# Kernel optimization log

Measured on AMD Instinct MI355X. Metric: run time of the kernel, lower is better.

## Reference

```python
import jax, jax.numpy as jnp
import numpy as np

B = 4096
DETER = 2048
BLOCKS = 8
HIDDEN = 256
SC, SD = 32, 16
STOCH = SC * SD  # 512
ACT = 17
EMBED = 1024
UNIMIX = 0.01
EPS = 1e-4
DPB = DETER // BLOCKS  # 256


def rmsnorm(x, scale):
    rms = jnp.sqrt(jnp.mean(x * x, axis=-1, keepdims=True) + EPS)
    return x / rms * scale


def dense(x, w, b):
    return x @ w + b


def block_linear(x, kernel, bias):
    # kernel: (out_per_block, in_per_block, blocks)
    bs = x.shape[:-1]
    ipb = x.shape[-1] // BLOCKS
    xg = x.reshape(*bs, BLOCKS, ipb)
    y = jnp.einsum('...gi,oig->...go', xg, kernel)
    return y.reshape(*bs, -1) + bias


def sample(logits):
    # unimix + straight-through argmax
    probs = jax.nn.softmax(logits, axis=-1)
    probs = (1.0 - UNIMIX) * probs + UNIMIX / SD
    logits = jnp.log(probs + 1e-8)
    soft = jax.nn.softmax(logits, axis=-1)
    hard = jax.nn.one_hot(jnp.argmax(logits, axis=-1), SD, dtype=soft.dtype)
    return hard + soft - jax.lax.stop_gradient(soft)


def setup_inputs() -> dict:
    key = jax.random.key(0)
    ks = jax.random.split(key, 16)

    def lecun(k, shape, fan_in):
        return jax.random.normal(k, shape, jnp.float32) / np.sqrt(fan_in)

    return {
        'stoch': jax.random.uniform(ks[0], (B, SC, SD), jnp.float32),
        'deter': jax.random.normal(ks[1], (B, DETER), jnp.float32),
        'action': jax.random.normal(ks[2], (B, ACT), jnp.float32),
        'embed': jax.random.normal(ks[3], (B, EMBED), jnp.float32),
        # Deter net params
        'in0_w': lecun(ks[4], (DETER, HIDDEN), DETER), 'in0_b': jnp.zeros((HIDDEN,)), 'in_norm0_s': jnp.ones((HIDDEN,)),
        'in1_w': lecun(ks[5], (STOCH, HIDDEN), STOCH), 'in1_b': jnp.zeros((HIDDEN,)), 'in_norm1_s': jnp.ones((HIDDEN,)),
        'in2_w': lecun(ks[6], (ACT, HIDDEN), ACT), 'in2_b': jnp.zeros((HIDDEN,)), 'in_norm2_s': jnp.ones((HIDDEN,)),
        'hid0_k': lecun(ks[7], (DPB, DPB + 3 * HIDDEN, BLOCKS), DPB + 3 * HIDDEN),
        'hid0_b': jnp.zeros((DETER,)), 'hid_norm0_s': jnp.ones((DETER,)),
        'gru_k': lecun(ks[8], (3 * DPB, DPB, BLOCKS), DPB), 'gru_b': jnp.zeros((3 * DETER,)),
        # posterior head
        'obs_fc0_w': lecun(ks[9], (DETER + EMBED, HIDDEN), DETER + EMBED), 'obs_fc0_b': jnp.zeros((HIDDEN,)),
        'obs_norm0_s': jnp.ones((HIDDEN,)),
        'obs_out_w': lecun(ks[10], (HIDDEN, STOCH), HIDDEN), 'obs_out_b': jnp.zeros((STOCH,)),
    }


def reference(stoch, deter, action, embed,
              in0_w, in0_b, in_norm0_s, in1_w, in1_b, in_norm1_s,
              in2_w, in2_b, in_norm2_s, hid0_k, hid0_b, hid_norm0_s,
              gru_k, gru_b, obs_fc0_w, obs_fc0_b, obs_norm0_s,
              obs_out_w, obs_out_b):
    Bn = stoch.shape[0]
    stoch_flat = stoch.reshape(Bn, -1)  # (B, 512)
    act = action / jnp.maximum(jnp.abs(action), 1.0)
    x0 = jax.nn.silu(rmsnorm(dense(deter, in0_w, in0_b), in_norm0_s))
    x1 = jax.nn.silu(rmsnorm(dense(stoch_flat, in1_w, in1_b), in_norm1_s))
    x2 = jax.nn.silu(rmsnorm(dense(act, in2_w, in2_b), in_norm2_s))
    x = jnp.concatenate([x0, x1, x2], axis=-1)  # (B, 768)
    x = jnp.broadcast_to(x[:, None, :], (Bn, BLOCKS, x.shape[-1]))
    deter_blocked = deter.reshape(Bn, BLOCKS, DPB)
    x = jnp.concatenate([deter_blocked, x], axis=-1).reshape(Bn, -1)  # (B, 8192)
    x = jax.nn.silu(rmsnorm(block_linear(x, hid0_k, hid0_b), hid_norm0_s))  # (B, 2048)
    gates = block_linear(x, gru_k, gru_b)  # (B, 6144)
    gates = gates.reshape(Bn, BLOCKS, 3 * DPB)
    g0, g1, g2 = jnp.split(gates, 3, axis=-1)
    reset = jax.nn.sigmoid(g0.reshape(Bn, -1))
    cand = g1.reshape(Bn, -1)
    update = jax.nn.sigmoid(g2.reshape(Bn, -1) - 1.0)
    new_deter = update * jnp.tanh(reset * cand) + (1.0 - update) * deter
    # posterior head
    h = jnp.concatenate([new_deter, embed], axis=-1)
    h = jax.nn.silu(rmsnorm(dense(h, obs_fc0_w, obs_fc0_b), obs_norm0_s))
    logit = dense(h, obs_out_w, obs_out_b).reshape(Bn, SC, SD)
    new_stoch = sample(logit)
    return (new_stoch, new_deter, logit)
```

## Files before the change

### kernel.cpp

```cpp
#include <hip/hip_runtime.h>
#include <cmath>

constexpr int BATCH = 4096;
constexpr float EPSN = 1e-4f;

constexpr int OFF_STOCH = 0;
constexpr int OFF_DETER = BATCH * 512;
constexpr int OFF_LOGIT = OFF_DETER + BATCH * 2048;

typedef unsigned short ushort;
typedef __attribute__((ext_vector_type(4))) float f32x4;
typedef __attribute__((ext_vector_type(8))) short s16x8;
struct us4 { ushort x, y, z, w; };

constexpr size_t U_WHH = 0;
constexpr size_t U_WHL = U_WHH + 2097152;
constexpr size_t U_WGH = U_WHL + 2097152;
constexpr size_t U_WGL = U_WGH + 1572864;
constexpr size_t U_WFH = U_WGL + 1572864;
constexpr size_t U_WFL = U_WFH + 786432;
constexpr size_t U_WOH = U_WFL + 786432;
constexpr size_t U_WOL = U_WOH + 131072;
constexpr size_t U_PEND = U_WOL + 131072;
constexpr size_t F_XB = U_PEND / 2;
constexpr size_t F_XH = F_XB + 3145728;
constexpr size_t U_X0H = (F_XH + 6291456) * 2;
constexpr size_t U_X0L = U_X0H + 524288;
constexpr size_t U_X1H = U_X0L + 524288;
constexpr size_t U_X1L = U_X1H + 131072;
constexpr size_t F_HB = F_XH + 4194304;

#define DINLINE __device__ __forceinline__

DINLINE float sigm(float x)  { return 1.0f / (1.0f + expf(-x)); }
DINLINE float siluf(float x) { return x / (1.0f + expf(-x)); }

DINLINE float4 ld4(const float* p) { return *reinterpret_cast<const float4*>(p); }
DINLINE void st4(float* p, float4 v) { *reinterpret_cast<float4*>(p) = v; }

DINLINE ushort f2bf(float x) {
  unsigned u = __float_as_uint(x);
  unsigned r = u + 0x7fffu + ((u >> 16) & 1u);
  return (ushort)(r >> 16);
}
DINLINE float bf2f(ushort h) { return __uint_as_float(((unsigned)h) << 16); }

DINLINE void cp16g(void* lds, const void* g) {
  __builtin_amdgcn_global_load_lds(
      (const __attribute__((address_space(1))) unsigned int*)g,
      (__attribute__((address_space(3))) unsigned int*)lds, 16, 0, 0);
}

DINLINE f32x4 mfma16(s16x8 a, s16x8 b, f32x4 c) {
  return __builtin_amdgcn_mfma_f32_16x16x32_bf16(a, b, c, 0, 0, 0);
}

DINLINE int swz_addr(int row, int kb0) {
  return (row * 64 + kb0) ^ ((row & 7) << 4);
}
DINLINE void dec_swz(int D, int& row, int& kb) {
  int r2 = (D >> 8) & 1;
  int r0 = ((D >> 6) & 1) ^ r2;
  row = ((D >> 7) << 1) | r0;
  kb = (D & 48) ^ ((row & 3) << 4);
}

DINLINE void split2(float x, ushort& h, ushort& l) {
  h = f2bf(x);
  l = f2bf(x - bf2f(h));
}

DINLINE float4 rms_silu4(float v0, float v1, float v2, float v3, float4 s4) {
  float ss = v0 * v0 + v1 * v1 + v2 * v2 + v3 * v3;
#pragma unroll
  for (int off = 32; off; off >>= 1) ss += __shfl_xor(ss, off);
  float inv = 1.0f / sqrtf(ss * (1.0f / 256.0f) + EPSN);
  float4 o;
  o.x = siluf(v0 * inv * s4.x); o.y = siluf(v1 * inv * s4.y);
  o.z = siluf(v2 * inv * s4.z); o.w = siluf(v3 * inv * s4.w);
  return o;
}

__global__ __launch_bounds__(256) void k_prep(
    const float* __restrict__ hk, const float* __restrict__ gk,
    const float* __restrict__ w0, const float* __restrict__ w1,
    const float* __restrict__ wf, const float* __restrict__ wo,
    ushort* __restrict__ wsU) {
  __shared__ float L[64 * 65];
  const int bid = blockIdx.x, tid = threadIdx.x;
  if (bid < 1792) {
    int t = bid * 256 + tid;
    const float* src; ushort* dh; ushort* dl; int e, plane;
    if (t < 262144) { e = t; src = hk + (size_t)e * 8; dh = wsU + U_WHH; dl = wsU + U_WHL; plane = 262144; }
    else { e = t - 262144; src = gk + (size_t)e * 8; dh = wsU + U_WGH; dl = wsU + U_WGL; plane = 196608; }
    float4 v0 = ld4(src), v1 = ld4(src + 4);
    float vv[8] = {v0.x, v0.y, v0.z, v0.w, v1.x, v1.y, v1.z, v1.w};
#pragma unroll
    for (int g2 = 0; g2 < 8; ++g2) {
      ushort h, l; split2(vv[g2], h, l);
      dh[(size_t)g2 * plane + e] = h;
      dl[(size_t)g2 * plane + e] = l;
    }
    return;
  }
  int t = bid - 1792;
  const float* src; ushort* dh; ushort* dl; int K, N;
  if (t < 128)      { src = w0; dh = wsU + U_X0H; dl = wsU + U_X0L; K = 2048; N = 256; }
  else if (t < 160) { t -= 128; src = w1; dh = wsU + U_X1H; dl = wsU + U_X1L; K = 512;  N = 256; }
  else if (t < 352) { t -= 160; src = wf; dh = wsU + U_WFH; dl = wsU + U_WFL; K = 3072; N = 256; }
  else              { t -= 352; src = wo; dh = wsU + U_WOH; dl = wsU + U_WOL; K = 256;  N = 512; }
  const int ntiles = N / 64;
  const int k0 = (t / ntiles) * 64, n0 = (t % ntiles) * 64;
#pragma unroll
  for (int q = 0; q < 4; ++q) {
    int row = q * 16 + (tid >> 4), col = (tid & 15) * 4;
    float4 v = ld4(src + (size_t)(k0 + row) * N + n0 + col);
    L[row * 65 + col]     = v.x;
    L[row * 65 + col + 1] = v.y;
    L[row * 65 + col + 2] = v.z;
    L[row * 65 + col + 3] = v.w;
  }
  __syncthreads();
  const int n = tid >> 2, kc = (tid & 3) * 16;
  s16x8 h0, h1, l0v, l1v;
#pragma unroll
  for (int j = 0; j < 16; ++j) {
    ushort h, l; split2(L[(kc + j) * 65 + n], h, l);
    if (j < 8) { h0[j] = (short)h; l0v[j] = (short)l; }
    else       { h1[j - 8] = (short)h; l1v[j - 8] = (short)l; }
  }
  size_t ob = (size_t)(n0 + n) * K + k0 + kc;
  *(s16x8*)(dh + ob)     = h0;
  *(s16x8*)(dh + ob + 8) = h1;
  *(s16x8*)(dl + ob)     = l0v;
  *(s16x8*)(dl + ob + 8) = l1v;
}

__global__ __launch_bounds__(512) void k_gemm256(
    int mode,
    const float* __restrict__ deter, const float* __restrict__ stoch,
    const float* __restrict__ newdet, const float* __restrict__ embed,
    const ushort* __restrict__ wsU, float* __restrict__ part) {
  __shared__ ushort Ah[2][64 * 32], Al[2][64 * 32];
  __shared__ ushort Wh[2][256 * 32], Wl[2][256 * 32];
  const int tid = threadIdx.x, lane = tid & 63, wv = tid >> 6;
  const int wr = wv >> 2, wc = wv & 3;
  const int bid = blockIdx.x;
  constexpr size_t PL0 = (size_t)4096 * 512;

  const float* A0; const float* A1 = nullptr;
  int lda0, lda1 = 0, ksw = 1 << 30;
  const ushort* whp; const ushort* wlp;
  int KwB, kbase, KT, m0, dstride, dcol;
  float* dst;

  if (mode == 0) {
    if (bid < 256) {
      int ks = bid & 3; m0 = (bid >> 2) * 64; kbase = ks * 512; KT = 16;
      A0 = deter; lda0 = 2048;
      whp = wsU + U_X0H; wlp = wsU + U_X0L; KwB = 4096;
      dst = part + (size_t)(ks >> 1) * PL0; dstride = 512; dcol = (ks & 1) * 256;
    } else {
      int b = bid - 256; int ks = b & 1; m0 = (b >> 1) * 64; kbase = ks * 256; KT = 8;
      A0 = stoch; lda0 = 512;
      whp = wsU + U_X1H; wlp = wsU + U_X1L; KwB = 1024;
      dst = part + 2 * PL0; dstride = 512; dcol = ks * 256;
    }
  } else {
    int ks = bid & 3; m0 = (bid >> 2) * 64; kbase = ks * 768; KT = 24;
    A0 = newdet; lda0 = 2048; A1 = embed; lda1 = 1024; ksw = 2048;
    whp = wsU + U_WFH; wlp = wsU + U_WFL; KwB = 6144;
    dst = part + (size_t)ks * 4096 * 256; dstride = 256; dcol = 0;
  }

  int wn0, wkb0, wn1, wkb1;
  dec_swz(tid * 16, wn0, wkb0);
  dec_swz(8192 + tid * 16, wn1, wkb1);
  const char* whB = (const char*)whp;
  const char* wlB = (const char*)wlp;
  const size_t wo0 = (size_t)wn0 * KwB + kbase * 2 + wkb0;
  const size_t wo1 = (size_t)wn1 * KwB + kbase * 2 + wkb1;

  const int arow = tid >> 2, akq = (tid & 3) * 8;
  const int abyte = swz_addr(arow, (tid & 3) * 16);
  float av[8];

  const f32x4 z4 = {0.f, 0.f, 0.f, 0.f};
  f32x4 acc[2][4];
#pragma unroll
  for (int i = 0; i < 2; ++i)
#pragma unroll
    for (int j = 0; j < 4; ++j) acc[i][j] = z4;

#define U_LOADA(kt) \
  if (tid < 256) { \
    int kg = kbase + (kt) * 32 + akq; \
    const float* p = (kg < ksw) ? A0 + (size_t)(m0 + arow) * lda0 + kg \
                                : A1 + (size_t)(m0 + arow) * lda1 + (kg - ksw); \
    float4 u_ = ld4(p), w_ = ld4(p + 4); \
    av[0] = u_.x; av[1] = u_.y; av[2] = u_.z; av[3] = u_.w; \
    av[4] = w_.x; av[5] = w_.y; av[6] = w_.z; av[7] = w_.w; \
  }
#define U_WRITEA(buf) \
  if (tid < 256) { \
    s16x8 h8, l8; \
    _Pragma("unroll") \
    for (int j = 0; j < 8; ++j) { \
      ushort h_, l_; split2(av[j], h_, l_); \
      h8[j] = (short)h_; l8[j] = (short)l_; \
    } \
    *(s16x8*)((char*)Ah[buf] + abyte) = h8; \
    *(s16x8*)((char*)Al[buf] + abyte) = l8; \
  }
#define U_ISSUEW(buf, kt) { \
    cp16g((char*)Wh[buf] + tid * 16, whB + wo0 + (kt) * 64); \
    cp16g((char*)Wh[buf] + 8192 + tid * 16, whB + wo1 + (kt) * 64); \
    cp16g((char*)Wl[buf] + tid * 16, wlB + wo0 + (kt) * 64); \
    cp16g((char*)Wl[buf] + 8192 + tid * 16, wlB + wo1 + (kt) * 64); \
  }

  U_LOADA(0);
  U_ISSUEW(0, 0);
  U_WRITEA(0);
  __syncthreads();
  int cur = 0;
  for (int t = 0; t < KT; ++t) {
    if (t + 1 < KT) { U_ISSUEW(cur ^ 1, t + 1); U_LOADA(t + 1); }
    const int k16 = (lane >> 4) * 16;
    s16x8 afh[2], afl[2];
#pragma unroll
    for (int mf = 0; mf < 2; ++mf) {
      int by = swz_addr(wr * 32 + mf * 16 + (lane & 15), k16);
      afh[mf] = *(const s16x8*)((const char*)Ah[cur] + by);
      afl[mf] = *(const s16x8*)((const char*)Al[cur] + by);
    }
#pragma unroll
    for (int nf = 0; nf < 4; ++nf) {
      int by = swz_addr(wc * 64 + nf * 16 + (lane & 15), k16);
      s16x8 bh = *(const s16x8*)((const char*)Wh[cur] + by);
      s16x8 bl = *(const s16x8*)((const char*)Wl[cur] + by);
#pragma unroll
      for (int mf = 0; mf < 2; ++mf) {
        acc[mf][nf] = mfma16(afh[mf], bh, acc[mf][nf]);
        acc[mf][nf] = mfma16(afh[mf], bl, acc[mf][nf]);
        acc[mf][nf] = mfma16(afl[mf], bh, acc[mf][nf]);
      }
    }
    if (t + 1 < KT) { U_WRITEA(cur ^ 1); }
    __syncthreads();
    cur ^= 1;
  }
#undef U_LOADA
#undef U_WRITEA
#undef U_ISSUEW
#pragma unroll
  for (int mf = 0; mf < 2; ++mf) {
    int rbase = m0 + wr * 32 + mf * 16 + ((lane >> 4) << 2);
#pragma unroll
    for (int nf = 0; nf < 4; ++nf) {
      int col = dcol + wc * 64 + nf * 16 + (lane & 15);
#pragma unroll
      for (int r = 0; r < 4; ++r)
        dst[(size_t)(rbase + r) * dstride + col] = acc[mf][nf][r];
    }
  }
}

__global__ __launch_bounds__(512) void k_x2(
    const float* __restrict__ action, const float* __restrict__ w2,
    const float* __restrict__ b2, const float* __restrict__ s2,
    ushort* __restrict__ xbp) {
  __shared__ float W2s[17 * 256];
  __shared__ float A2s[128 * 20];
  const int tid = threadIdx.x, tx = tid & 63, wv = tid >> 6;
  const int m0 = blockIdx.x * 128;
  for (int e = tid; e < 17 * 256; e += 512) W2s[e] = w2[e];
  for (int e = tid; e < 128 * 17; e += 512) {
    int r = e / 17, c = e % 17;
    float a = action[(size_t)(m0 + r) * 17 + c];
    float m = fabsf(a);
    A2s[r * 20 + c] = a / (m > 1.f ? m : 1.f);
  }
  __syncthreads();
  float4 acc2[16];
#pragma unroll
  for (int r = 0; r < 16; ++r) acc2[r] = make_float4(0.f, 0.f, 0.f, 0.f);
#pragma unroll
  for (int k = 0; k < 17; ++k) {
    float4 w4 = ld4(W2s + k * 256 + tx * 4);
#pragma unroll
    for (int r = 0; r < 16; ++r) {
      float av = A2s[(wv * 16 + r) * 20 + k];
      acc2[r].x = fmaf(av, w4.x, acc2[r].x);
      acc2[r].y = fmaf(av, w4.y, acc2[r].y);
      acc2[r].z = fmaf(av, w4.z, acc2[r].z);
      acc2[r].w = fmaf(av, w4.w, acc2[r].w);
    }
  }
  float4 b4 = ld4(b2 + tx * 4);
  float4 s4 = ld4(s2 + tx * 4);
#pragma unroll
  for (int r = 0; r < 16; ++r) {
    float4 o = rms_silu4(acc2[r].x + b4.x, acc2[r].y + b4.y,
                         acc2[r].z + b4.z, acc2[r].w + b4.w, s4);
    us4 h4, l4;
    split2(o.x, h4.x, l4.x); split2(o.y, h4.y, l4.y);
    split2(o.z, h4.z, l4.z); split2(o.w, h4.w, l4.w);
    size_t rb = (size_t)(m0 + wv * 16 + r) * 1536;
    *(us4*)(xbp + rb + 512 + tx * 4) = h4;
    *(us4*)(xbp + rb + 768 + 512 + tx * 4) = l4;
  }
}

__global__ __launch_bounds__(256) void k_comb_in(
    const float* __restrict__ part,
    const float* __restrict__ b0, const float* __restrict__ s0,
    const float* __restrict__ b1, const float* __restrict__ s1,
    ushort* __restrict__ xbp) {
  const int tid = threadIdx.x, tx = tid & 63, wv = tid >> 6;
  const size_t row = blockIdx.x * 2 + (wv >> 1);
  const int half = wv & 1;
  constexpr size_t PL = (size_t)4096 * 512;
  float4 v = make_float4(0.f, 0.f, 0.f, 0.f);
  if (half == 0) {
#pragma unroll
    for (int p = 0; p < 2; ++p) {
      const float* s = part + p * PL + row * 512 + tx * 4;
      float4 a = ld4(s), b = ld4(s + 256);
      v.x += a.x + b.x; v.y += a.y + b.y; v.z += a.z + b.z; v.w += a.w + b.w;
    }
  } else {
    const float* s = part + 2 * PL + row * 512 + tx * 4;
    float4 a = ld4(s), b = ld4(s + 256);
    v.x = a.x + b.x; v.y = a.y + b.y; v.z = a.z + b.z; v.w = a.w + b.w;
  }
  const float* bp = half ? b1 : b0;
  const float* sp = half ? s1 : s0;
  float4 b4 = ld4(bp + tx * 4);
  float4 s4 = ld4(sp + tx * 4);
  float4 o = rms_silu4(v.x + b4.x, v.y + b4.y, v.z + b4.z, v.w + b4.w, s4);
  us4 h4, l4;
  split2(o.x, h4.x, l4.x); split2(o.y, h4.y, l4.y);
  split2(o.z, h4.z, l4.z); split2(o.w, h4.w, l4.w);
  *(us4*)(xbp + row * 1536 + half * 256 + tx * 4) = h4;
  *(us4*)(xbp + row * 1536 + 768 + half * 256 + tx * 4) = l4;
}

__global__ __launch_bounds__(256) void k_comb4(
    const float* __restrict__ part, const float* __restrict__ bias,
    const float* __restrict__ scale, ushort* __restrict__ hbp) {
  const int tid = threadIdx.x, tx = tid & 63, wv = tid >> 6;
  const size_t row = blockIdx.x * 4 + wv;
  float4 v = make_float4(0.f, 0.f, 0.f, 0.f);
#pragma unroll
  for (int ks = 0; ks < 4; ++ks) {
    float4 t = ld4(part + (size_t)ks * 4096 * 256 + row * 256 + tx * 4);
    v.x += t.x; v.y += t.y; v.z += t.z; v.w += t.w;
  }
  float4 b4 = ld4(bias + tx * 4);
  float4 s4 = ld4(scale + tx * 4);
  float4 o = rms_silu4(v.x + b4.x, v.y + b4.y, v.z + b4.z, v.w + b4.w, s4);
  us4 h4, l4;
  split2(o.x, h4.x, l4.x); split2(o.y, h4.y, l4.y);
  split2(o.z, h4.z, l4.z); split2(o.w, h4.w, l4.w);
  *(us4*)(hbp + row * 512 + tx * 4) = h4;
  *(us4*)(hbp + row * 512 + 256 + tx * 4) = l4;
}

__global__ __launch_bounds__(512) void k_hid0m(
    const float* __restrict__ deter, const ushort* __restrict__ xbp,
    const ushort* __restrict__ wsU,
    const float* __restrict__ hbias, float* __restrict__ yh) {
  __shared__ ushort Ah[2][64 * 32], Al[2][64 * 32];
  __shared__ ushort Wh[2][256 * 32], Wl[2][256 * 32];
  const int tid = threadIdx.x, lane = tid & 63, wv = tid >> 6;
  const int wr = wv >> 2, wc = wv & 3;
  const int g = blockIdx.x & 7;
  const int m0 = (int)(blockIdx.x >> 3) * 64;

  int wn0, wkb0, wn1, wkb1;
  dec_swz(tid * 16, wn0, wkb0);
  dec_swz(8192 + tid * 16, wn1, wkb1);
  const char* whhB = (const char*)(wsU + U_WHH) + (size_t)g * 256 * 2048;
  const char* whlB = (const char*)(wsU + U_WHL) + (size_t)g * 256 * 2048;
  const char* xbB = (const char*)xbp;

  const int arow = tid >> 2, akq = (tid & 3) * 8;
  const int abyte = swz_addr(arow, (tid & 3) * 16);
  int an0, akb;
  dec_swz(tid * 16, an0, akb);
  float av[8];

  const f32x4 z4 = {0.f, 0.f, 0.f, 0.f};
  f32x4 acc[2][4];
#pragma unroll
  for (int i = 0; i < 2; ++i)
#pragma unroll
    for (int j = 0; j < 4; ++j) acc[i][j] = z4;

#define H_LOADA_DET(kt) \
  if (tid < 256) { \
    const float* p = deter + (size_t)(m0 + arow) * 2048 + g * 256 + (kt) * 32 + akq; \
    float4 u_ = ld4(p), w_ = ld4(p + 4); \
    av[0] = u_.x; av[1] = u_.y; av[2] = u_.z; av[3] = u_.w; \
    av[4] = w_.x; av[5] = w_.y; av[6] = w_.z; av[7] = w_.w; \
  }
#define H_WRITEA(buf) \
  if (tid < 256) { \
    s16x8 h8, l8; \
    _Pragma("unroll") \
    for (int j = 0; j < 8; ++j) { \
      ushort h_, l_; split2(av[j], h_, l_); \
      h8[j] = (short)h_; l8[j] = (short)l_; \
    } \
    *(s16x8*)((char*)Ah[buf] + abyte) = h8; \
    *(s16x8*)((char*)Al[buf] + abyte) = l8; \
  }
#define H_ISSUEA(buf, kt) \
  if (tid < 256) { \
    size_t rb = (size_t)(m0 + an0) * 3072; \
    int co = ((kt) * 32 - 256) * 2 + akb; \
    cp16g((char*)Ah[buf] + tid * 16, xbB + rb + co); \
    cp16g((char*)Al[buf] + tid * 16, xbB + rb + 1536 + co); \
  }
#define H_ISSUEW(buf, kt) { \
    size_t o0_ = (size_t)wn0 * 2048 + (kt) * 64 + wkb0; \
    size_t o1_ = (size_t)wn1 * 2048 + (kt) * 64 + wkb1; \
    cp16g((char*)Wh[buf] + tid * 16, whhB + o0_); \
    cp16g((char*)Wh[buf] + 8192 + tid * 16, whhB + o1_); \
    cp16g((char*)Wl[buf] + tid * 16, whlB + o0_); \
    cp16g((char*)Wl[buf] + 8192 + tid * 16, whlB + o1_); \
  }

  H_LOADA_DET(0);
  H_ISSUEW(0, 0);
  H_WRITEA(0);
  __syncthreads();
  int cur = 0;
  for (int t = 0; t < 32; ++t) {
    const bool pf = (t + 1 < 32);
    const bool det = (t + 1 < 8);
    if (pf) {
      H_ISSUEW(cur ^ 1, t + 1);
      if (det) { H_LOADA_DET(t + 1); }
      else     { H_ISSUEA(cur ^ 1, t + 1); }
    }
    const int k16 = (lane >> 4) * 16;
    s16x8 afh[2], afl[2];
#pragma unroll
    for (int mf = 0; mf < 2; ++mf) {
      int by = swz_addr(wr * 32 + mf * 16 + (lane & 15), k16);
      afh[mf] = *(const s16x8*)((const char*)Ah[cur] + by);
      afl[mf] = *(const s16x8*)((const char*)Al[cur] + by);
    }
#pragma unroll
    for (int nf = 0; nf < 4; ++nf) {
      int by = swz_addr(wc * 64 + nf * 16 + (lane & 15), k16);
      s16x8 bh = *(const s16x8*)((const char*)Wh[cur] + by);
      s16x8 bl = *(const s16x8*)((const char*)Wl[cur] + by);
#pragma unroll
      for (int mf = 0; mf < 2; ++mf) {
        acc[mf][nf] = mfma16(afh[mf], bh, acc[mf][nf]);
        acc[mf][nf] = mfma16(afh[mf], bl, acc[mf][nf]);
        acc[mf][nf] = mfma16(afl[mf], bh, acc[mf][nf]);
      }
    }
    if (pf && det) { H_WRITEA(cur ^ 1); }
    __syncthreads();
    cur ^= 1;
  }
#undef H_LOADA_DET
#undef H_WRITEA
#undef H_ISSUEA
#undef H_ISSUEW
#pragma unroll
  for (int mf = 0; mf < 2; ++mf) {
    int rbase = m0 + wr * 32 + mf * 16 + ((lane >> 4) << 2);
#pragma unroll
    for (int nf = 0; nf < 4; ++nf) {
      int col = wc * 64 + nf * 16 + (lane & 15);
      float b = hbias[g * 256 + col];
#pragma unroll
      for (int r = 0; r < 4; ++r)
        yh[(size_t)(rbase + r) * 2048 + g * 256 + col] = acc[mf][nf][r] + b;
    }
  }
}

__global__ __launch_bounds__(256) void k_rmsnorm2048(
    float* __restrict__ xh, const float* __restrict__ scale) {
  const int b = blockIdx.x, tid = threadIdx.x;
  float* row = xh + (size_t)b * 2048;
  float4 v0 = ld4(row + tid * 8);
  float4 v1 = ld4(row + tid * 8 + 4);
  float ss = v0.x * v0.x + v0.y * v0.y + v0.z * v0.z + v0.w * v0.w +
             v1.x * v1.x + v1.y * v1.y + v1.z * v1.z + v1.w * v1.w;
#pragma unroll
  for (int off = 32; off; off >>= 1) ss += __shfl_xor(ss, off);
  __shared__ float wsum[4];
  if ((tid & 63) == 0) wsum[tid >> 6] = ss;
  __syncthreads();
  float tot = wsum[0] + wsum[1] + wsum[2] + wsum[3];
  float inv = 1.0f / sqrtf(tot * (1.0f / 2048.0f) + EPSN);
  float4 sc0 = ld4(scale + tid * 8);
  float4 sc1 = ld4(scale + tid * 8 + 4);
  float o[8];
  o[0] = siluf(v0.x * inv * sc0.x); o[1] = siluf(v0.y * inv * sc0.y);
  o[2] = siluf(v0.z * inv * sc0.z); o[3] = siluf(v0.w * inv * sc0.w);
  o[4] = siluf(v1.x * inv * sc1.x); o[5] = siluf(v1.y * inv * sc1.y);
  o[6] = siluf(v1.z * inv * sc1.z); o[7] = siluf(v1.w * inv * sc1.w);
  s16x8 h8, l8;
#pragma unroll
  for (int j = 0; j < 8; ++j) {
    ushort h, l; split2(o[j], h, l);
    h8[j] = (short)h; l8[j] = (short)l;
  }
  ushort* rp = (ushort*)row;
  *(s16x8*)(rp + tid * 8) = h8;
  *(s16x8*)(rp + 2048 + tid * 8) = l8;
}

__global__ __launch_bounds__(512) void k_grum(
    const ushort* __restrict__ xhp, const ushort* __restrict__ wsU,
    const float* __restrict__ gb, const float* __restrict__ deter,
    float* __restrict__ newdet) {
  __shared__ ushort Ah[2][128 * 32], Al[2][128 * 32];
  __shared__ ushort Wh[2][192 * 32], Wl[2][192 * 32];
  const int tid = threadIdx.x, lane = tid & 63, wv = tid >> 6;
  const int wr = wv >> 2, wc = wv & 3;
  const int g = blockIdx.x & 7;
  const int nc = (int)(blockIdx.x >> 3) & 3;
  const int m0 = (int)(blockIdx.x >> 5) * 128;

  int wn0, wkb0, wn1, wkb1;
  dec_swz(tid * 16, wn0, wkb0);
  dec_swz(8192 + tid * 16, wn1, wkb1);
  const char* wghB = (const char*)(wsU + U_WGH);
  const char* wglB = (const char*)(wsU + U_WGL);
  const size_t wo0 = (size_t)(g * 768 + ((wn0 >> 6) << 8) + nc * 64 + (wn0 & 63)) * 512 + wkb0;
  const size_t wo1 = (size_t)(g * 768 + ((wn1 >> 6) << 8) + nc * 64 + (wn1 & 63)) * 512 + wkb1;

  const char* xhB = (const char*)xhp;
  int an0, akb;
  dec_swz(tid * 16, an0, akb);

  const f32x4 z4 = {0.f, 0.f, 0.f, 0.f};
  f32x4 acc[4][3];
#pragma unroll
  for (int i = 0; i < 4; ++i)
#pragma unroll
    for (int j = 0; j < 3; ++j) acc[i][j] = z4;

#define G_ISSUEA(buf, kt) { \
    size_t rb = (size_t)(m0 + an0) * 8192; \
    int co = (g * 256 + (kt) * 32) * 2 + akb; \
    cp16g((char*)Ah[buf] + tid * 16, xhB + rb + co); \
    cp16g((char*)Al[buf] + tid * 16, xhB + rb + 4096 + co); \
  }
#define G_ISSUEW(buf, kt) { \
    cp16g((char*)Wh[buf] + tid * 16, wghB + wo0 + (kt) * 64); \
    cp16g((char*)Wl[buf] + tid * 16, wglB + wo0 + (kt) * 64); \
    if (tid < 256) { \
      cp16g((char*)Wh[buf] + 8192 + tid * 16, wghB + wo1 + (kt) * 64); \
      cp16g((char*)Wl[buf] + 8192 + tid * 16, wglB + wo1 + (kt) * 64); \
    } }

  G_ISSUEW(0, 0);
  G_ISSUEA(0, 0);
  __syncthreads();
  int cur = 0;
  for (int t = 0; t < 8; ++t) {
    if (t + 1 < 8) { G_ISSUEW(cur ^ 1, t + 1); G_ISSUEA(cur ^ 1, t + 1); }
    const int k16 = (lane >> 4) * 16;
    s16x8 afh[4], afl[4];
#pragma unroll
    for (int mf = 0; mf < 4; ++mf) {
      int by = swz_addr(wr * 64 + mf * 16 + (lane & 15), k16);
      afh[mf] = *(const s16x8*)((const char*)Ah[cur] + by);
      afl[mf] = *(const s16x8*)((const char*)Al[cur] + by);
    }
#pragma unroll
    for (int gt = 0; gt < 3; ++gt) {
      int by = swz_addr(gt * 64 + wc * 16 + (lane & 15), k16);
      s16x8 bh = *(const s16x8*)((const char*)Wh[cur] + by);
      s16x8 bl = *(const s16x8*)((const char*)Wl[cur] + by);
#pragma unroll
      for (int mf = 0; mf < 4; ++mf) {
        acc[mf][gt] = mfma16(afh[mf], bh, acc[mf][gt]);
        acc[mf][gt] = mfma16(afh[mf], bl, acc[mf][gt]);
        acc[mf][gt] = mfma16(afl[mf], bh, acc[mf][gt]);
      }
    }
    __syncthreads();
    cur ^= 1;
  }
#undef G_ISSUEA
#undef G_ISSUEW
  const int col = nc * 64 + wc * 16 + (lane & 15);
  const float br = gb[g * 768 + col];
  const float bc = gb[g * 768 + 256 + col];
  const float bu = gb[g * 768 + 512 + col];
#pragma unroll
  for (int mf = 0; mf < 4; ++mf) {
    int rbase = m0 + wr * 64 + mf * 16 + ((lane >> 4) << 2);
#pragma unroll
    for (int r = 0; r < 4; ++r) {
      int row = rbase + r;
      float rr = sigm(acc[mf][0][r] + br);
      float cc = acc[mf][1][r] + bc;
      float uu = sigm(acc[mf][2][r] + bu - 1.0f);
      float d = deter[(size_t)row * 2048 + g * 256 + col];
      newdet[(size_t)row * 2048 + g * 256 + col] =
          uu * tanhf(rr * cc) + (1.0f - uu) * d;
    }
  }
}

__global__ __launch_bounds__(512) void k_obsoutm(
    const ushort* __restrict__ hbp, const ushort* __restrict__ wsU,
    const float* __restrict__ ob, float* __restrict__ logit) {
  __shared__ ushort Ah[2][64 * 32], Al[2][64 * 32];
  __shared__ ushort Wh[2][256 * 32], Wl[2][256 * 32];
  const int tid = threadIdx.x, lane = tid & 63, wv = tid >> 6;
  const int wr = wv >> 2, wc = wv & 3;
  const int half = blockIdx.x & 1;
  const int m0 = (int)(blockIdx.x >> 1) * 64;

  int wn0, wkb0, wn1, wkb1;
  dec_swz(tid * 16, wn0, wkb0);
  dec_swz(8192 + tid * 16, wn1, wkb1);
  const char* whB = (const char*)(wsU + U_WOH) + (size_t)half * 256 * 512;
  const char* wlB = (const char*)(wsU + U_WOL) + (size_t)half * 256 * 512;
  const size_t wo0 = (size_t)wn0 * 512 + wkb0;
  const size_t wo1 = (size_t)wn1 * 512 + wkb1;

  const char* hbB = (const char*)hbp;
  int an0, akb;
  dec_swz(tid * 16, an0, akb);

  const f32x4 z4 = {0.f, 0.f, 0.f, 0.f};
  f32x4 acc[2][4];
#pragma unroll
  for (int i = 0; i < 2; ++i)
#pragma unroll
    for (int j = 0; j < 4; ++j) acc[i][j] = z4;

#define O_ISSUEA(buf, kt) \
  if (tid < 256) { \
    size_t rb = (size_t)(m0 + an0) * 1024; \
    int co = (kt) * 64 + akb; \
    cp16g((char*)Ah[buf] + tid * 16, hbB + rb + co); \
    cp16g((char*)Al[buf] + tid * 16, hbB + rb + 512 + co); \
  }
#define O_ISSUEW(buf, kt) { \
    cp16g((char*)Wh[buf] + tid * 16, whB + wo0 + (kt) * 64); \
    cp16g((char*)Wh[buf] + 8192 + tid * 16, whB + wo1 + (kt) * 64); \
    cp16g((char*)Wl[buf] + tid * 16, wlB + wo0 + (kt) * 64); \
    cp16g((char*)Wl[buf] + 8192 + tid * 16, wlB + wo1 + (kt) * 64); \
  }

  O_ISSUEW(0, 0);
  O_ISSUEA(0, 0);
  __syncthreads();
  int cur = 0;
  for (int t = 0; t < 8; ++t) {
    if (t + 1 < 8) { O_ISSUEW(cur ^ 1, t + 1); O_ISSUEA(cur ^ 1, t + 1); }
    const int k16 = (lane >> 4) * 16;
    s16x8 afh[2], afl[2];
#pragma unroll
    for (int mf = 0; mf < 2; ++mf) {
      int by = swz_addr(wr * 32 + mf * 16 + (lane & 15), k16);
      afh[mf] = *(const s16x8*)((const char*)Ah[cur] + by);
      afl[mf] = *(const s16x8*)((const char*)Al[cur] + by);
    }
#pragma unroll
    for (int nf = 0; nf < 4; ++nf) {
      int by = swz_addr(wc * 64 + nf * 16 + (lane & 15), k16);
      s16x8 bh = *(const s16x8*)((const char*)Wh[cur] + by);
      s16x8 bl = *(const s16x8*)((const char*)Wl[cur] + by);
#pragma unroll
      for (int mf = 0; mf < 2; ++mf) {
        acc[mf][nf] = mfma16(afh[mf], bh, acc[mf][nf]);
        acc[mf][nf] = mfma16(afh[mf], bl, acc[mf][nf]);
        acc[mf][nf] = mfma16(afl[mf], bh, acc[mf][nf]);
      }
    }
    __syncthreads();
    cur ^= 1;
  }
#undef O_ISSUEA
#undef O_ISSUEW
#pragma unroll
  for (int mf = 0; mf < 2; ++mf) {
    int rbase = m0 + wr * 32 + mf * 16 + ((lane >> 4) << 2);
#pragma unroll
    for (int nf = 0; nf < 4; ++nf) {
      int col = half * 256 + wc * 64 + nf * 16 + (lane & 15);
      float b = ob[col];
#pragma unroll
      for (int r = 0; r < 4; ++r)
        logit[(size_t)(rbase + r) * 512 + col] = acc[mf][nf][r] + b;
    }
  }
}

__global__ __launch_bounds__(256) void k_argmax(
    const float* __restrict__ logit, float* __restrict__ stoch_out) {
  const size_t row = blockIdx.x * 4 + (threadIdx.x >> 6);
  const int lane = threadIdx.x & 63;
  const float* lp = logit + row * 512 + lane * 8;
  float4 a = ld4(lp), b = ld4(lp + 4);
  float v[8] = {a.x, a.y, a.z, a.w, b.x, b.y, b.z, b.w};
  float bv = v[0]; int bi = 0;
#pragma unroll
  for (int j = 1; j < 8; ++j)
    if (v[j] > bv) { bv = v[j]; bi = j; }
  bi += lane * 8;
  float pv = __shfl_xor(bv, 1);
  int   pi = __shfl_xor(bi, 1);
  if (pv > bv || (pv == bv && pi < bi)) { bv = pv; bi = pi; }
  float4 o0, o1;
  int base = lane * 8;
  o0.x = (bi == base + 0) ? 1.f : 0.f;
  o0.y = (bi == base + 1) ? 1.f : 0.f;
  o0.z = (bi == base + 2) ? 1.f : 0.f;
  o0.w = (bi == base + 3) ? 1.f : 0.f;
  o1.x = (bi == base + 4) ? 1.f : 0.f;
  o1.y = (bi == base + 5) ? 1.f : 0.f;
  o1.z = (bi == base + 6) ? 1.f : 0.f;
  o1.w = (bi == base + 7) ? 1.f : 0.f;
  st4(stoch_out + row * 512 + base, o0);
  st4(stoch_out + row * 512 + base + 4, o1);
}

extern "C" void kernel_launch(void* const* d_in, const int* in_sizes, int n_in,
                              void* d_out, int out_size, void* d_ws, size_t ws_size,
                              hipStream_t stream) {
  (void)in_sizes; (void)n_in; (void)out_size; (void)ws_size;
  const float* stoch      = (const float*)d_in[0];
  const float* deter      = (const float*)d_in[1];
  const float* action     = (const float*)d_in[2];
  const float* embed      = (const float*)d_in[3];
  const float* in0_w      = (const float*)d_in[4];
  const float* in0_b      = (const float*)d_in[5];
  const float* n0_s       = (const float*)d_in[6];
  const float* in1_w      = (const float*)d_in[7];
  const float* in1_b      = (const float*)d_in[8];
  const float* n1_s       = (const float*)d_in[9];
  const float* in2_w      = (const float*)d_in[10];
  const float* in2_b      = (const float*)d_in[11];
  const float* n2_s       = (const float*)d_in[12];
  const float* hid0_k     = (const float*)d_in[13];
  const float* hid0_b     = (const float*)d_in[14];
  const float* hidn_s     = (const float*)d_in[15];
  const float* gru_k      = (const float*)d_in[16];
  const float* gru_b      = (const float*)d_in[17];
  const float* obs_fc0_w  = (const float*)d_in[18];
  const float* obs_fc0_b  = (const float*)d_in[19];
  const float* obs_n_s    = (const float*)d_in[20];
  const float* obs_out_w  = (const float*)d_in[21];
  const float* obs_out_b  = (const float*)d_in[22];

  float*  out = (float*)d_out;
  float*  ws  = (float*)d_ws;
  ushort* wsU = (ushort*)d_ws;
  ushort* xbp = (ushort*)(ws + F_XB);
  float*  xh  = ws + F_XH;
  ushort* xhp = (ushort*)(ws + F_XH);
  ushort* hbp = (ushort*)(ws + F_HB);
  float*  part = xh;

  hipLaunchKernelGGL(k_prep, dim3(2176), dim3(256), 0, stream,
                     hid0_k, gru_k, in0_w, in1_w, obs_fc0_w, obs_out_w, wsU);
  hipLaunchKernelGGL(k_x2, dim3(32), dim3(512), 0, stream,
                     action, in2_w, in2_b, n2_s, xbp);
  hipLaunchKernelGGL(k_gemm256, dim3(384), dim3(512), 0, stream,
                     0, deter, stoch, out + OFF_DETER, embed, wsU, part);
  hipLaunchKernelGGL(k_comb_in, dim3(2048), dim3(256), 0, stream,
                     part, in0_b, n0_s, in1_b, n1_s, xbp);
  hipLaunchKernelGGL(k_hid0m, dim3(512), dim3(512), 0, stream,
                     deter, xbp, wsU, hid0_b, xh);
  hipLaunchKernelGGL(k_rmsnorm2048, dim3(4096), dim3(256), 0, stream, xh, hidn_s);
  hipLaunchKernelGGL(k_grum, dim3(1024), dim3(512), 0, stream,
                     xhp, wsU, gru_b, deter, out + OFF_DETER);
  hipLaunchKernelGGL(k_gemm256, dim3(256), dim3(512), 0, stream,
                     1, deter, stoch, out + OFF_DETER, embed, wsU, part);
  hipLaunchKernelGGL(k_comb4, dim3(1024), dim3(256), 0, stream,
                     part, obs_fc0_b, obs_n_s, hbp);
  hipLaunchKernelGGL(k_obsoutm, dim3(128), dim3(512), 0, stream,
                     hbp, wsU, obs_out_b, out + OFF_LOGIT);
  hipLaunchKernelGGL(k_argmax, dim3(1024), dim3(256), 0, stream,
                     out + OFF_LOGIT, out + OFF_STOCH);
}
```

Before: 241.2 us.

## Pre-swizzle weights into MFMA fragment order and load B directly from global

The prep kernel now writes all bf16 hi/lo weight planes in an MFMA-fragment-major layout, so each lane's 16-byte B fragment sits contiguously in global memory. The GEMM kernels drop the shared-memory weight staging buffers and async copies and load B fragments straight into registers each k-step. This removes LDS traffic and shrinks shared memory use, which may raise occupancy. In exchange, weight loads are no longer double-buffered ahead of use, so global/L2 latency may show up inside the MFMA loop.

Measured after the change: 258.1 us. 7.0% more time.

```diff
diff --git a/kernel.cpp b/kernel.cpp
--- a/kernel.cpp
+++ b/kernel.cpp
@@ -70,6 +70,10 @@
   l = f2bf(x - bf2f(h));
 }
 
+DINLINE size_t frag_idx(int n, int k, int NK) {
+  return ((size_t)((n >> 4) * NK + (k >> 5)) * 64 + ((k >> 3) & 3) * 16 + (n & 15)) * 8 + (k & 7);
+}
+
 DINLINE float4 rms_silu4(float v0, float v1, float v2, float v3, float4 s4) {
   float ss = v0 * v0 + v1 * v1 + v2 * v2 + v3 * v3;
 #pragma unroll
@@ -90,16 +94,33 @@
   const int bid = blockIdx.x, tid = threadIdx.x;
   if (bid < 1792) {
     int t = bid * 256 + tid;
-    const float* src; ushort* dh; ushort* dl; int e, plane;
-    if (t < 262144) { e = t; src = hk + (size_t)e * 8; dh = wsU + U_WHH; dl = wsU + U_WHL; plane = 262144; }
-    else { e = t - 262144; src = gk + (size_t)e * 8; dh = wsU + U_WGH; dl = wsU + U_WGL; plane = 196608; }
-    float4 v0 = ld4(src), v1 = ld4(src + 4);
-    float vv[8] = {v0.x, v0.y, v0.z, v0.w, v1.x, v1.y, v1.z, v1.w};
-#pragma unroll
-    for (int g2 = 0; g2 < 8; ++g2) {
-      ushort h, l; split2(vv[g2], h, l);
-      dh[(size_t)g2 * plane + e] = h;
-      dl[(size_t)g2 * plane + e] = l;
+    if (t < 262144) {
+      int o = t >> 10, i = t & 1023;
+      const float* src = hk + (size_t)t * 8;
+      float4 v0 = ld4(src), v1 = ld4(src + 4);
+      float vv[8] = {v0.x, v0.y, v0.z, v0.w, v1.x, v1.y, v1.z, v1.w};
+      size_t fi = frag_idx(o, i, 32);
+#pragma unroll
+      for (int g2 = 0; g2 < 8; ++g2) {
+        ushort h, l; split2(vv[g2], h, l);
+        wsU[U_WHH + (size_t)g2 * 262144 + fi] = h;
+        wsU[U_WHL + (size_t)g2 * 262144 + fi] = l;
+      }
+    } else {
+      int e = t - 262144;
+      int o = e >> 8, i = e & 255;
+      const float* src = gk + (size_t)e * 8;
+      float4 v0 = ld4(src), v1 = ld4(src + 4);
+      float vv[8] = {v0.x, v0.y, v0.z, v0.w, v1.x, v1.y, v1.z, v1.w};
+      int gate = o >> 8, nc = (o >> 6) & 3, srow = gate * 64 + (o & 63);
+      size_t fi = frag_idx(srow, i, 8);
+#pragma unroll
+      for (int g2 = 0; g2 < 8; ++g2) {
+        ushort h, l; split2(vv[g2], h, l);
+        size_t pb = (size_t)(g2 * 4 + nc) * 49152;
+        wsU[U_WGH + pb + fi] = h;
+        wsU[U_WGL + pb + fi] = l;
+      }
     }
     return;
   }
@@ -109,6 +130,7 @@
   else if (t < 160) { t -= 128; src = w1; dh = wsU + U_X1H; dl = wsU + U_X1L; K = 512;  N = 256; }
   else if (t < 352) { t -= 160; src = wf; dh = wsU + U_WFH; dl = wsU + U_WFL; K = 3072; N = 256; }
   else              { t -= 352; src = wo; dh = wsU + U_WOH; dl = wsU + U_WOL; K = 256;  N = 512; }
+  const int NK = K / 32;
   const int ntiles = N / 64;
   const int k0 = (t / ntiles) * 64, n0 = (t % ntiles) * 64;
 #pragma unroll
@@ -121,19 +143,21 @@
     L[row * 65 + col + 3] = v.w;
   }
   __syncthreads();
-  const int n = tid >> 2, kc = (tid & 3) * 16;
+  const int nl = tid >> 2, kc = (tid & 3) * 16;
+  const int ng = n0 + nl;
   s16x8 h0, h1, l0v, l1v;
 #pragma unroll
   for (int j = 0; j < 16; ++j) {
-    ushort h, l; split2(L[(kc + j) * 65 + n], h, l);
+    ushort h, l; split2(L[(kc + j) * 65 + nl], h, l);
     if (j < 8) { h0[j] = (short)h; l0v[j] = (short)l; }
     else       { h1[j - 8] = (short)h; l1v[j - 8] = (short)l; }
   }
-  size_t ob = (size_t)(n0 + n) * K + k0 + kc;
-  *(s16x8*)(dh + ob)     = h0;
-  *(s16x8*)(dh + ob + 8) = h1;
-  *(s16x8*)(dl + ob)     = l0v;
-  *(s16x8*)(dl + ob + 8) = l1v;
+  size_t fa = frag_idx(ng, k0 + kc, NK);
+  size_t fb = frag_idx(ng, k0 + kc + 8, NK);
+  *(s16x8*)(dh + fa) = h0;
+  *(s16x8*)(dh + fb) = h1;
+  *(s16x8*)(dl + fa) = l0v;
+  *(s16x8*)(dl + fb) = l1v;
 }
 
 __global__ __launch_bounds__(512) void k_gemm256(
@@ -142,7 +166,6 @@
     const float* __restrict__ newdet, const float* __restrict__ embed,
     const ushort* __restrict__ wsU, float* __restrict__ part) {
   __shared__ ushort Ah[2][64 * 32], Al[2][64 * 32];
-  __shared__ ushort Wh[2][256 * 32], Wl[2][256 * 32];
   const int tid = threadIdx.x, lane = tid & 63, wv = tid >> 6;
   const int wr = wv >> 2, wc = wv & 3;
   const int bid = blockIdx.x;
@@ -150,36 +173,28 @@
 
   const float* A0; const float* A1 = nullptr;
   int lda0, lda1 = 0, ksw = 1 << 30;
-  const ushort* whp; const ushort* wlp;
-  int KwB, kbase, KT, m0, dstride, dcol;
+  const ushort* wFh; const ushort* wFl;
+  int NKt, kch0, kbase, KT, m0, dstride, dcol;
   float* dst;
 
   if (mode == 0) {
     if (bid < 256) {
       int ks = bid & 3; m0 = (bid >> 2) * 64; kbase = ks * 512; KT = 16;
       A0 = deter; lda0 = 2048;
-      whp = wsU + U_X0H; wlp = wsU + U_X0L; KwB = 4096;
+      wFh = wsU + U_X0H; wFl = wsU + U_X0L; NKt = 64; kch0 = ks * 16;
       dst = part + (size_t)(ks >> 1) * PL0; dstride = 512; dcol = (ks & 1) * 256;
     } else {
       int b = bid - 256; int ks = b & 1; m0 = (b >> 1) * 64; kbase = ks * 256; KT = 8;
       A0 = stoch; lda0 = 512;
-      whp = wsU + U_X1H; wlp = wsU + U_X1L; KwB = 1024;
+      wFh = wsU + U_X1H; wFl = wsU + U_X1L; NKt = 16; kch0 = ks * 8;
       dst = part + 2 * PL0; dstride = 512; dcol = ks * 256;
     }
   } else {
     int ks = bid & 3; m0 = (bid >> 2) * 64; kbase = ks * 768; KT = 24;
     A0 = newdet; lda0 = 2048; A1 = embed; lda1 = 1024; ksw = 2048;
-    whp = wsU + U_WFH; wlp = wsU + U_WFL; KwB = 6144;
+    wFh = wsU + U_WFH; wFl = wsU + U_WFL; NKt = 96; kch0 = ks * 24;
     dst = part + (size_t)ks * 4096 * 256; dstride = 256; dcol = 0;
   }
-
-  int wn0, wkb0, wn1, wkb1;
-  dec_swz(tid * 16, wn0, wkb0);
-  dec_swz(8192 + tid * 16, wn1, wkb1);
-  const char* whB = (const char*)whp;
-  const char* wlB = (const char*)wlp;
-  const size_t wo0 = (size_t)wn0 * KwB + kbase * 2 + wkb0;
-  const size_t wo1 = (size_t)wn1 * KwB + kbase * 2 + wkb1;
 
   const int arow = tid >> 2, akq = (tid & 3) * 8;
   const int abyte = swz_addr(arow, (tid & 3) * 16);
@@ -212,20 +227,20 @@
     *(s16x8*)((char*)Ah[buf] + abyte) = h8; \
     *(s16x8*)((char*)Al[buf] + abyte) = l8; \
   }
-#define U_ISSUEW(buf, kt) { \
-    cp16g((char*)Wh[buf] + tid * 16, whB + wo0 + (kt) * 64); \
-    cp16g((char*)Wh[buf] + 8192 + tid * 16, whB + wo1 + (kt) * 64); \
-    cp16g((char*)Wl[buf] + tid * 16, wlB + wo0 + (kt) * 64); \
-    cp16g((char*)Wl[buf] + 8192 + tid * 16, wlB + wo1 + (kt) * 64); \
-  }
 
   U_LOADA(0);
-  U_ISSUEW(0, 0);
   U_WRITEA(0);
   __syncthreads();
   int cur = 0;
   for (int t = 0; t < KT; ++t) {
-    if (t + 1 < KT) { U_ISSUEW(cur ^ 1, t + 1); U_LOADA(t + 1); }
+    if (t + 1 < KT) { U_LOADA(t + 1); }
+    s16x8 bh[4], bl[4];
+#pragma unroll
+    for (int nf = 0; nf < 4; ++nf) {
+      size_t fo = ((size_t)((wc * 4 + nf) * NKt + kch0 + t) * 64 + lane) * 8;
+      bh[nf] = *(const s16x8*)(wFh + fo);
+      bl[nf] = *(const s16x8*)(wFl + fo);
+    }
     const int k16 = (lane >> 4) * 16;
     s16x8 afh[2], afl[2];
 #pragma unroll
@@ -236,14 +251,11 @@
     }
 #pragma unroll
     for (int nf = 0; nf < 4; ++nf) {
-      int by = swz_addr(wc * 64 + nf * 16 + (lane & 15), k16);
-      s16x8 bh = *(const s16x8*)((const char*)Wh[cur] + by);
-      s16x8 bl = *(const s16x8*)((const char*)Wl[cur] + by);
 #pragma unroll
       for (int mf = 0; mf < 2; ++mf) {
-        acc[mf][nf] = mfma16(afh[mf], bh, acc[mf][nf]);
-        acc[mf][nf] = mfma16(afh[mf], bl, acc[mf][nf]);
-        acc[mf][nf] = mfma16(afl[mf], bh, acc[mf][nf]);
+        acc[mf][nf] = mfma16(afh[mf], bh[nf], acc[mf][nf]);
+        acc[mf][nf] = mfma16(afh[mf], bl[nf], acc[mf][nf]);
+        acc[mf][nf] = mfma16(afl[mf], bh[nf], acc[mf][nf]);
       }
     }
     if (t + 1 < KT) { U_WRITEA(cur ^ 1); }
@@ -252,7 +264,6 @@
   }
 #undef U_LOADA
 #undef U_WRITEA
-#undef U_ISSUEW
 #pragma unroll
   for (int mf = 0; mf < 2; ++mf) {
     int rbase = m0 + wr * 32 + mf * 16 + ((lane >> 4) << 2);
@@ -372,17 +383,13 @@
     const ushort* __restrict__ wsU,
     const float* __restrict__ hbias, float* __restrict__ yh) {
   __shared__ ushort Ah[2][64 * 32], Al[2][64 * 32];
-  __shared__ ushort Wh[2][256 * 32], Wl[2][256 * 32];
   const int tid = threadIdx.x, lane = tid & 63, wv = tid >> 6;
   const int wr = wv >> 2, wc = wv & 3;
   const int g = blockIdx.x & 7;
   const int m0 = (int)(blockIdx.x >> 3) * 64;
 
-  int wn0, wkb0, wn1, wkb1;
-  dec_swz(tid * 16, wn0, wkb0);
-  dec_swz(8192 + tid * 16, wn1, wkb1);
-  const char* whhB = (const char*)(wsU + U_WHH) + (size_t)g * 256 * 2048;
-  const char* whlB = (const char*)(wsU + U_WHL) + (size_t)g * 256 * 2048;
+  const ushort* whFh = wsU + U_WHH + (size_t)g * 262144;
+  const ushort* whFl = wsU + U_WHL + (size_t)g * 262144;
   const char* xbB = (const char*)xbp;
 
   const int arow = tid >> 2, akq = (tid & 3) * 8;
@@ -423,17 +430,8 @@
     cp16g((char*)Ah[buf] + tid * 16, xbB + rb + co); \
     cp16g((char*)Al[buf] + tid * 16, xbB + rb + 1536 + co); \
   }
-#define H_ISSUEW(buf, kt) { \
-    size_t o0_ = (size_t)wn0 * 2048 + (kt) * 64 + wkb0; \
-    size_t o1_ = (size_t)wn1 * 2048 + (kt) * 64 + wkb1; \
-    cp16g((char*)Wh[buf] + tid * 16, whhB + o0_); \
-    cp16g((char*)Wh[buf] + 8192 + tid * 16, whhB + o1_); \
-    cp16g((char*)Wl[buf] + tid * 16, whlB + o0_); \
-    cp16g((char*)Wl[buf] + 8192 + tid * 16, whlB + o1_); \
-  }
 
   H_LOADA_DET(0);
-  H_ISSUEW(0, 0);
   H_WRITEA(0);
   __syncthreads();
   int cur = 0;
@@ -441,9 +439,15 @@
     const bool pf = (t + 1 < 32);
     const bool det = (t + 1 < 8);
     if (pf) {
-      H_ISSUEW(cur ^ 1, t + 1);
       if (det) { H_LOADA_DET(t + 1); }
       else     { H_ISSUEA(cur ^ 1, t + 1); }
+    }
+    s16x8 bh[4], bl[4];
+#pragma unroll
+    for (int nf = 0; nf < 4; ++nf) {
+      size_t fo = ((size_t)((wc * 4 + nf) * 32 + t) * 64 + lane) * 8;
+      bh[nf] = *(const s16x8*)(whFh + fo);
+      bl[nf] = *(const s16x8*)(whFl + fo);
     }
     const int k16 = (lane >> 4) * 16;
     s16x8 afh[2], afl[2];
@@ -455,14 +459,11 @@
     }
 #pragma unroll
     for (int nf = 0; nf < 4; ++nf) {
-      int by = swz_addr(wc * 64 + nf * 16 + (lane & 15), k16);
-      s16x8 bh = *(const s16x8*)((const char*)Wh[cur] + by);
-      s16x8 bl = *(const s16x8*)((const char*)Wl[cur] + by);
 #pragma unroll
       for (int mf = 0; mf < 2; ++mf) {
-        acc[mf][nf] = mfma16(afh[mf], bh, acc[mf][nf]);
-        acc[mf][nf] = mfma16(afh[mf], bl, acc[mf][nf]);
-        acc[mf][nf] = mfma16(afl[mf], bh, acc[mf][nf]);
+        acc[mf][nf] = mfma16(afh[mf], bh[nf], acc[mf][nf]);
+        acc[mf][nf] = mfma16(afh[mf], bl[nf], acc[mf][nf]);
+        acc[mf][nf] = mfma16(afl[mf], bh[nf], acc[mf][nf]);
       }
     }
     if (pf && det) { H_WRITEA(cur ^ 1); }
@@ -472,7 +473,6 @@
 #undef H_LOADA_DET
 #undef H_WRITEA
 #undef H_ISSUEA
-#undef H_ISSUEW
 #pragma unroll
   for (int mf = 0; mf < 2; ++mf) {
     int rbase = m0 + wr * 32 + mf * 16 + ((lane >> 4) << 2);
@@ -525,20 +525,14 @@
     const float* __restrict__ gb, const float* __restrict__ deter,
     float* __restrict__ newdet) {
   __shared__ ushort Ah[2][128 * 32], Al[2][128 * 32];
-  __shared__ ushort Wh[2][192 * 32], Wl[2][192 * 32];
   const int tid = threadIdx.x, lane = tid & 63, wv = tid >> 6;
   const int wr = wv >> 2, wc = wv & 3;
   const int g = blockIdx.x & 7;
   const int nc = (int)(blockIdx.x >> 3) & 3;
   const int m0 = (int)(blockIdx.x >> 5) * 128;
 
-  int wn0, wkb0, wn1, wkb1;
-  dec_swz(tid * 16, wn0, wkb0);
-  dec_swz(8192 + tid * 16, wn1, wkb1);
-  const char* wghB = (const char*)(wsU + U_WGH);
-  const char* wglB = (const char*)(wsU + U_WGL);
-  const size_t wo0 = (size_t)(g * 768 + ((wn0 >> 6) << 8) + nc * 64 + (wn0 & 63)) * 512 + wkb0;
-  const size_t wo1 = (size_t)(g * 768 + ((wn1 >> 6) << 8) + nc * 64 + (wn1 & 63)) * 512 + wkb1;
+  const ushort* wgFh = wsU + U_WGH + (size_t)(g * 4 + nc) * 49152;
+  const ushort* wgFl = wsU + U_WGL + (size_t)(g * 4 + nc) * 49152;
 
   const char* xhB = (const char*)xhp;
   int an0, akb;
@@ -557,20 +551,19 @@
     cp16g((char*)Ah[buf] + tid * 16, xhB + rb + co); \
     cp16g((char*)Al[buf] + tid * 16, xhB + rb + 4096 + co); \
   }
-#define G_ISSUEW(buf, kt) { \
-    cp16g((char*)Wh[buf] + tid * 16, wghB + wo0 + (kt) * 64); \
-    cp16g((char*)Wl[buf] + tid * 16, wglB + wo0 + (kt) * 64); \
-    if (tid < 256) { \
-      cp16g((char*)Wh[buf] + 8192 + tid * 16, wghB + wo1 + (kt) * 64); \
-      cp16g((char*)Wl[buf] + 8192 + tid * 16, wglB + wo1 + (kt) * 64); \
-    } }
-
-  G_ISSUEW(0, 0);
+
   G_ISSUEA(0, 0);
   __syncthreads();
   int cur = 0;
   for (int t = 0; t < 8; ++t) {
-    if (t + 1 < 8) { G_ISSUEW(cur ^ 1, t + 1); G_ISSUEA(cur ^ 1, t + 1); }
+    if (t + 1 < 8) { G_ISSUEA(cur ^ 1, t + 1); }
+    s16x8 bh[3], bl[3];
+#pragma unroll
+    for (int gt = 0; gt < 3; ++gt) {
+      size_t fo = ((size_t)((gt * 4 + wc) * 8 + t) * 64 + lane) * 8;
+      bh[gt] = *(const s16x8*)(wgFh + fo);
+      bl[gt] = *(const s16x8*)(wgFl + fo);
+    }
     const int k16 = (lane >> 4) * 16;
     s16x8 afh[4], afl[4];
 #pragma unroll
@@ -581,21 +574,17 @@
     }
 #pragma unroll
     for (int gt = 0; gt < 3; ++gt) {
-      int by = swz_addr(gt * 64 + wc * 16 + (lane & 15), k16);
-      s16x8 bh = *(const s16x8*)((const char*)Wh[cur] + by);
-      s16x8 bl = *(const s16x8*)((const char*)Wl[cur] + by);
 #pragma unroll
       for (int mf = 0; mf < 4; ++mf) {
-        acc[mf][gt] = mfma16(afh[mf], bh, acc[mf][gt]);
-        acc[mf][gt] = mfma16(afh[mf], bl, acc[mf][gt]);
-        acc[mf][gt] = mfma16(afl[mf], bh, acc[mf][gt]);
+        acc[mf][gt] = mfma16(afh[mf], bh[gt], acc[mf][gt]);
+        acc[mf][gt] = mfma16(afh[mf], bl[gt], acc[mf][gt]);
+        acc[mf][gt] = mfma16(afl[mf], bh[gt], acc[mf][gt]);
       }
     }
     __syncthreads();
     cur ^= 1;
   }
 #undef G_ISSUEA
-#undef G_ISSUEW
   const int col = nc * 64 + wc * 16 + (lane & 15);
   const float br = gb[g * 768 + col];
   const float bc = gb[g * 768 + 256 + col];
@@ -620,20 +609,13 @@
     const ushort* __restrict__ hbp, const ushort* __restrict__ wsU,
     const float* __restrict__ ob, float* __restrict__ logit) {
   __shared__ ushort Ah[2][64 * 32], Al[2][64 * 32];
-  __shared__ ushort Wh[2][256 * 32], Wl[2][256 * 32];
   const int tid = threadIdx.x, lane = tid & 63, wv = tid >> 6;
   const int wr = wv >> 2, wc = wv & 3;
   const int half = blockIdx.x & 1;
   const int m0 = (int)(blockIdx.x >> 1) * 64;
 
-  int wn0, wkb0, wn1, wkb1;
-  dec_swz(tid * 16, wn0, wkb0);
-  dec_swz(8192 + tid * 16, wn1, wkb1);
-  const char* whB = (const char*)(wsU + U_WOH) + (size_t)half * 256 * 512;
-  const char* wlB = (const char*)(wsU + U_WOL) + (size_t)half * 256 * 512;
-  const size_t wo0 = (size_t)wn0 * 512 + wkb0;
-  const size_t wo1 = (size_t)wn1 * 512 + wkb1;
-
+  const ushort* woFh = wsU + U_WOH;
+  const ushort* woFl = wsU + U_WOL;
   const char* hbB = (const char*)hbp;
   int an0, akb;
   dec_swz(tid * 16, an0, akb);
@@ -652,19 +634,19 @@
     cp16g((char*)Ah[buf] + tid * 16, hbB + rb + co); \
     cp16g((char*)Al[buf] + tid * 16, hbB + rb + 512 + co); \
   }
-#define O_ISSUEW(buf, kt) { \
-    cp16g((char*)Wh[buf] + tid * 16, whB + wo0 + (kt) * 64); \
-    cp16g((char*)Wh[buf] + 8192 + tid * 16, whB + wo1 + (kt) * 64); \
-    cp16g((char*)Wl[buf] + tid * 16, wlB + wo0 + (kt) * 64); \
-    cp16g((char*)Wl[buf] + 8192 + tid * 16, wlB + wo1 + (kt) * 64); \
-  }
-
-  O_ISSUEW(0, 0);
+
   O_ISSUEA(0, 0);
   __syncthreads();
   int cur = 0;
   for (int t = 0; t < 8; ++t) {
-    if (t + 1 < 8) { O_ISSUEW(cur ^ 1, t + 1); O_ISSUEA(cur ^ 1, t + 1); }
+    if (t + 1 < 8) { O_ISSUEA(cur ^ 1, t + 1); }
+    s16x8 bh[4], bl[4];
+#pragma unroll
+    for (int nf = 0; nf < 4; ++nf) {
+      size_t fo = ((size_t)((half * 16 + wc * 4 + nf) * 8 + t) * 64 + lane) * 8;
+      bh[nf] = *(const s16x8*)(woFh + fo);
+      bl[nf] = *(const s16x8*)(woFl + fo);
+    }
     const int k16 = (lane >> 4) * 16;
     s16x8 afh[2], afl[2];
 #pragma unroll
@@ -675,21 +657,17 @@
     }
 #pragma unroll
     for (int nf = 0; nf < 4; ++nf) {
-      int by = swz_addr(wc * 64 + nf * 16 + (lane & 15), k16);
-      s16x8 bh = *(const s16x8*)((const char*)Wh[cur] + by);
-      s16x8 bl = *(const s16x8*)((const char*)Wl[cur] + by);
 #pragma unroll
       for (int mf = 0; mf < 2; ++mf) {
-        acc[mf][nf] = mfma16(afh[mf], bh, acc[mf][nf]);
-        acc[mf][nf] = mfma16(afh[mf], bl, acc[mf][nf]);
-        acc[mf][nf] = mfma16(afl[mf], bh, acc[mf][nf]);
+        acc[mf][nf] = mfma16(afh[mf], bh[nf], acc[mf][nf]);
+        acc[mf][nf] = mfma16(afh[mf], bl[nf], acc[mf][nf]);
+        acc[mf][nf] = mfma16(afl[mf], bh[nf], acc[mf][nf]);
       }
     }
     __syncthreads();
     cur ^= 1;
   }
 #undef O_ISSUEA
-#undef O_ISSUEW
 #pragma unroll
   for (int mf = 0; mf < 2; ++mf) {
     int rbase = m0 + wr * 32 + mf * 16 + ((lane >> 4) << 2);
```
